# Performance work log

Measured on AMD Instinct MI355X. Metric: run time of the kernel, lower is better.

## Reference

```python
import jax, jax.numpy as jnp
import numpy as np

INPUT_DIM = 64

def setup_inputs() -> dict:
    key = jax.random.key(0)
    k1, k2, k3 = jax.random.split(key, 3)
    B, Lq, Lk, D = 4, 4096, 4096, INPUT_DIM
    return {
        "query": jax.random.normal(k1, (B, Lq, D), dtype=jnp.float32),
        "keys": jax.random.normal(k2, (B, Lk, D), dtype=jnp.float32),
        "values": jax.random.normal(k3, (B, Lk, D), dtype=jnp.float32),
    }

def reference(query, keys, values):
    scale = 1.0 / jnp.sqrt(jnp.asarray(INPUT_DIM, dtype=jnp.float32))
    # scores: [B, Lq, Lk]
    scores = jnp.einsum("bqd,bkd->bqk", query, keys) * scale
    attn = jax.nn.softmax(scores, axis=-1)
    # output: [B, Lq, D]
    return jnp.einsum("bqk,bkd->bqd", attn, values)
```

## Files before the change

kernel.cpp:

```cpp
#include <hip/hip_runtime.h>
#include <hip/hip_bf16.h>

typedef __bf16 bf16x8 __attribute__((ext_vector_type(8)));
typedef float  f32x4  __attribute__((ext_vector_type(4)));

#define LQ 4096
#define LKK 4096
#define DH 64
#define KBLK 64
#define QBLK 64
#define NIT (LKK / KBLK)
#define NB 4
#define GR_TILE 512
#define ARR_ELEMS ((size_t)NB * NIT * GR_TILE * 8)
#define KV_BYTES (4 * ARR_ELEMS * sizeof(__bf16))
#define PO_BYTES ((size_t)512 * 4096 * sizeof(float))
#define PML_BYTES ((size_t)512 * 128 * sizeof(float))
#define WS_SPLIT (KV_BYTES + PO_BYTES + PML_BYTES)
#define WS_SINGLE KV_BYTES

union BFU { unsigned short u; __bf16 b; };
__device__ __forceinline__ __bf16 u2bf(unsigned short v) { BFU x; x.u = v; return x.b; }
__device__ __forceinline__ unsigned short bf2u(__bf16 b) { BFU x; x.b = b; return x.u; }

typedef const __attribute__((address_space(1))) void* gas1_t;
typedef __attribute__((address_space(3))) void* las3_t;
__device__ __forceinline__ void gload_lds16(const void* g, void* l) {
    __builtin_amdgcn_global_load_lds((gas1_t)g, (las3_t)l, 16, 0, 0);
}

__device__ __forceinline__ unsigned cvt_pk_bf16(float a, float b) {
    unsigned r;
    asm volatile("v_cvt_pk_bf16_f32 %0, %1, %2" : "=v"(r) : "v"(a), "v"(b));
    return r;
}


__global__ __launch_bounds__(256)
void prepack(const float* __restrict__ Kg, const float* __restrict__ Vg,
             __bf16* __restrict__ ws)
{
    __bf16* KHI = ws;
    __bf16* KLO = ws + ARR_ELEMS;
    __bf16* VHI = ws + 2 * ARR_ELEMS;
    __bf16* VLO = ws + 3 * ARR_ELEMS;

    const int gid = blockIdx.x * 256 + threadIdx.x;
    const int isV = gid >> 17;
    const int t   = gid & 131071;
    const int b   = t >> 15;
    const int rem = t & 32767;
    const int kt  = rem >> 9;
    const int G   = rem & 511;
    const int blk = G >> 7;
    const int c   = (G >> 6) & 1;
    const int gg  = (G >> 4) & 3;
    const int ll  = G & 15;

    const size_t dst = ((size_t)(b * NIT + kt) * GR_TILE + G) * 8;
    float x[8];
    if (!isV) {
        const float* src = Kg + ((size_t)b * LKK + kt * KBLK + 16 * blk + ll) * DH + 32 * c + 8 * gg;
        float4 a0 = *(const float4*)src;
        float4 a1 = *(const float4*)(src + 4);
        x[0]=a0.x; x[1]=a0.y; x[2]=a0.z; x[3]=a0.w;
        x[4]=a1.x; x[5]=a1.y; x[6]=a1.z; x[7]=a1.w;
        bf16x8 h, l;
#pragma unroll
        for (int j = 0; j < 8; ++j) {
            __bf16 hh = (__bf16)x[j];
            h[j] = hh; l[j] = (__bf16)(x[j] - (float)hh);
        }
        *(bf16x8*)&KHI[dst] = h;  *(bf16x8*)&KLO[dst] = l;
    } else {
        const float* src = Vg + ((size_t)b * LKK + kt * KBLK + 32 * c + 8 * gg) * DH + 16 * blk + ll;
#pragma unroll
        for (int j = 0; j < 8; ++j) x[j] = src[(size_t)j * DH];
        bf16x8 h, l;
#pragma unroll
        for (int j = 0; j < 8; ++j) {
            __bf16 hh = (__bf16)x[j];
            h[j] = hh; l[j] = (__bf16)(x[j] - (float)hh);
        }
        *(bf16x8*)&VHI[dst] = h;  *(bf16x8*)&VLO[dst] = l;
    }
}

__global__ __launch_bounds__(256, 2)
void attn_split(const float* __restrict__ Qg, const __bf16* __restrict__ ws,
                float* __restrict__ PO, float* __restrict__ PML)
{
    const int bid = blockIdx.x;
    const int h   = bid & 1;
    const int bz  = (bid >> 1) & 3;
    const int qt  = bid >> 3;
    const int pb  = h * 256 + bz * 64 + qt;
    const int tid  = threadIdx.x;
    const int w    = tid >> 6;
    const int lane = tid & 63;
    const int g    = lane >> 4;
    const int l15  = lane & 15;
    const int q0   = qt * QBLK + w * 16;

    __shared__ __align__(16) __bf16 TILES[2][4][GR_TILE * 8];
    __shared__ __align__(16) unsigned int PSM[4][16 * 64];

    const __bf16* wsA[4] = { ws, ws + ARR_ELEMS, ws + 2 * ARR_ELEMS, ws + 3 * ARR_ELEMS };
    const size_t bqoff = (size_t)bz * LQ * DH;

    bf16x8 qhi[2], qlo[2];
#pragma unroll
    for (int c = 0; c < 2; ++c) {
        const float* src = Qg + bqoff + (size_t)(q0 + l15) * DH + 32 * c + 8 * g;
#pragma unroll
        for (int j = 0; j < 8; ++j) {
            float x = src[j] * 0.125f;
            __bf16 hh = (__bf16)x;
            qhi[c][j] = hh;
            qlo[c][j] = (__bf16)(x - (float)hh);
        }
    }

    auto STAGE = [&](int buf, int kt) {
        const size_t toff = (size_t)(bz * NIT + kt) * GR_TILE * 8;
#pragma unroll
        for (int a = 0; a < 4; ++a) {
            const __bf16* src = wsA[a] + toff + (size_t)(w * 128 + lane) * 8;
            __bf16* dst = &TILES[buf][a][w * 128 * 8];
            gload_lds16(src, dst);
            gload_lds16(src + 64 * 8, dst + 64 * 8);
        }
    };

    f32x4 oacc[4] = {};
    float m_run = -1e30f, l_run = 0.f;

    const int kt0 = h * (NIT / 2);
    STAGE(0, kt0);
    __syncthreads();

    int cur = 0;
    const int sw = (l15 & 7) << 2;
    const int prow = l15 * 64;

    for (int it = 0; it < NIT / 2; ++it) {
        if (it + 1 < NIT / 2) STAGE(cur ^ 1, kt0 + it + 1);

        const __bf16* KHI_l = TILES[cur][0];
        const __bf16* KLO_l = TILES[cur][1];
        const __bf16* VHI_l = TILES[cur][2];
        const __bf16* VLO_l = TILES[cur][3];

        f32x4 s[4] = {};
        __builtin_amdgcn_s_setprio(1);
#pragma unroll
        for (int kb = 0; kb < 4; ++kb) {
#pragma unroll
            for (int c = 0; c < 2; ++c) {
                bf16x8 kh = *(const bf16x8*)&KHI_l[((kb * 2 + c) * 64 + lane) * 8];
                bf16x8 kl = *(const bf16x8*)&KLO_l[((kb * 2 + c) * 64 + lane) * 8];
                s[kb] = __builtin_amdgcn_mfma_f32_16x16x32_bf16(kh, qhi[c], s[kb], 0, 0, 0);
                s[kb] = __builtin_amdgcn_mfma_f32_16x16x32_bf16(kh, qlo[c], s[kb], 0, 0, 0);
                s[kb] = __builtin_amdgcn_mfma_f32_16x16x32_bf16(kl, qhi[c], s[kb], 0, 0, 0);
            }
        }
        __builtin_amdgcn_s_setprio(0);

        float tmax = -1e30f;
#pragma unroll
        for (int kb = 0; kb < 4; ++kb)
#pragma unroll
            for (int r = 0; r < 4; ++r)
                tmax = fmaxf(tmax, s[kb][r]);
        tmax = fmaxf(tmax, __shfl_xor(tmax, 16, 64));
        tmax = fmaxf(tmax, __shfl_xor(tmax, 32, 64));

        const bool defer = __all(tmax <= m_run + 8.f);
        float alpha = 1.f;
        if (!defer) {
            float mnew = fmaxf(m_run, tmax);
            alpha = __expf(m_run - mnew);
            m_run = mnew;
        }

        float psum = 0.f;
#pragma unroll
        for (int kb = 0; kb < 4; ++kb)
#pragma unroll
            for (int r = 0; r < 4; ++r) {
                float p = __expf(s[kb][r] - m_run);
                s[kb][r] = p;
                psum += p;
            }
        psum += __shfl_xor(psum, 16, 64);
        psum += __shfl_xor(psum, 32, 64);

        if (!defer) {
            l_run = l_run * alpha + psum;
#pragma unroll
            for (int db = 0; db < 4; ++db) oacc[db] *= alpha;
        } else {
            l_run += psum;
        }

#pragma unroll
        for (int kb = 0; kb < 4; ++kb) {
            unsigned h0 = cvt_pk_bf16(s[kb][0], s[kb][1]);
            unsigned h1 = cvt_pk_bf16(s[kb][2], s[kb][3]);
            float l0 = s[kb][0] - __uint_as_float(h0 << 16);
            float l1 = s[kb][1] - __uint_as_float(h0 & 0xffff0000u);
            float l2 = s[kb][2] - __uint_as_float(h1 << 16);
            float l3 = s[kb][3] - __uint_as_float(h1 & 0xffff0000u);
            unsigned lo0 = cvt_pk_bf16(l0, l1);
            unsigned lo1 = cvt_pk_bf16(l2, l3);
            const int wb = 8 * kb + 2 * g;
            PSM[w][prow + ((wb)     ^ sw)]      = h0;
            PSM[w][prow + ((wb + 1) ^ sw)]      = h1;
            PSM[w][prow + 32 + ((wb)     ^ sw)] = lo0;
            PSM[w][prow + 32 + ((wb + 1) ^ sw)] = lo1;
        }

#pragma unroll
        for (int c = 0; c < 2; ++c) {
            const int qb = prow + (((4 * c + g) ^ (l15 & 7)) << 2);
            bf16x8 ph = *(const bf16x8*)&PSM[w][qb];
            bf16x8 pl = *(const bf16x8*)&PSM[w][qb + 32];
            __builtin_amdgcn_s_setprio(1);
#pragma unroll
            for (int db = 0; db < 4; ++db) {
                bf16x8 vh = *(const bf16x8*)&VHI_l[((db * 2 + c) * 64 + lane) * 8];
                bf16x8 vl = *(const bf16x8*)&VLO_l[((db * 2 + c) * 64 + lane) * 8];
                oacc[db] = __builtin_amdgcn_mfma_f32_16x16x32_bf16(vh, ph, oacc[db], 0, 0, 0);
                oacc[db] = __builtin_amdgcn_mfma_f32_16x16x32_bf16(vl, ph, oacc[db], 0, 0, 0);
                oacc[db] = __builtin_amdgcn_mfma_f32_16x16x32_bf16(vh, pl, oacc[db], 0, 0, 0);
            }
            __builtin_amdgcn_s_setprio(0);
        }

        __syncthreads();
        cur ^= 1;
    }

    float* po = PO + (size_t)pb * (QBLK * DH) + (size_t)(w * 16 + l15) * DH;
#pragma unroll
    for (int db = 0; db < 4; ++db)
        *(f32x4*)&po[16 * db + 4 * g] = oacc[db];
    if (g == 0) {
        PML[pb * 128 + w * 16 + l15]      = m_run;
        PML[pb * 128 + 64 + w * 16 + l15] = l_run;
    }
}

__global__ __launch_bounds__(256)
void combine(const float* __restrict__ PO, const float* __restrict__ PML,
             float* __restrict__ Og)
{
    const int t  = blockIdx.x * 256 + threadIdx.x;
    const int d   = t & 63;
    const int row = (t >> 6) & 4095;
    const int bz  = t >> 18;
    const int qt  = row >> 6, ri = row & 63;
    const int pb0 = bz * 64 + qt;
    const int pb1 = 256 + pb0;
    float m0 = PML[pb0 * 128 + ri], l0 = PML[pb0 * 128 + 64 + ri];
    float m1 = PML[pb1 * 128 + ri], l1 = PML[pb1 * 128 + 64 + ri];
    float M  = fmaxf(m0, m1);
    float a0 = __expf(m0 - M), a1 = __expf(m1 - M);
    float o0 = PO[(size_t)pb0 * 4096 + ri * 64 + d];
    float o1 = PO[(size_t)pb1 * 4096 + ri * 64 + d];
    Og[t] = (a0 * o0 + a1 * o1) / (a0 * l0 + a1 * l1);
}

__global__ __launch_bounds__(256, 1)
void attn_fwd_pre(const float* __restrict__ Qg, const __bf16* __restrict__ ws,
                  float* __restrict__ Og)
{
    const int bid = blockIdx.x;
    const int bz  = (bid >> 1) & 3;
    const int qt  = ((bid & 1) << 5) | (bid >> 3);
    const int tid  = threadIdx.x;
    const int w    = tid >> 6;
    const int lane = tid & 63;
    const int g    = lane >> 4;
    const int l15  = lane & 15;
    const int q0   = qt * QBLK + w * 16;

    __shared__ __align__(16) __bf16 TILES[2][4][GR_TILE * 8];
    __shared__ __align__(16) unsigned int PSM[4][16 * 64];

    const __bf16* wsA[4] = { ws, ws + ARR_ELEMS, ws + 2 * ARR_ELEMS, ws + 3 * ARR_ELEMS };
    const size_t bqoff = (size_t)bz * LQ * DH;

    bf16x8 qhi[2], qlo[2];
#pragma unroll
    for (int c = 0; c < 2; ++c) {
        const float* src = Qg + bqoff + (size_t)(q0 + l15) * DH + 32 * c + 8 * g;
#pragma unroll
        for (int j = 0; j < 8; ++j) {
            float x = src[j] * 0.125f;
            __bf16 hh = (__bf16)x;
            qhi[c][j] = hh;
            qlo[c][j] = (__bf16)(x - (float)hh);
        }
    }

    auto STAGE = [&](int buf, int kt) {
        const size_t toff = (size_t)(bz * NIT + kt) * GR_TILE * 8;
#pragma unroll
        for (int a = 0; a < 4; ++a) {
            const __bf16* src = wsA[a] + toff + (size_t)(w * 128 + lane) * 8;
            __bf16* dst = &TILES[buf][a][w * 128 * 8];
            gload_lds16(src, dst);
            gload_lds16(src + 64 * 8, dst + 64 * 8);
        }
    };

    f32x4 oacc[4] = {};
    float m_run[4], l_run[4];
#pragma unroll
    for (int r = 0; r < 4; ++r) { m_run[r] = -1e30f; l_run[r] = 0.f; }

    STAGE(0, 0);
    __syncthreads();

    int cur = 0;
    for (int kt = 0; kt < NIT; ++kt) {
        if (kt + 1 < NIT) STAGE(cur ^ 1, kt + 1);

        const __bf16* KHI_l = TILES[cur][0];
        const __bf16* KLO_l = TILES[cur][1];
        const __bf16* VHI_l = TILES[cur][2];
        const __bf16* VLO_l = TILES[cur][3];

        f32x4 s[4] = {};
#pragma unroll
        for (int kb = 0; kb < 4; ++kb) {
#pragma unroll
            for (int c = 0; c < 2; ++c) {
                bf16x8 kh = *(const bf16x8*)&KHI_l[((kb * 2 + c) * 64 + lane) * 8];
                bf16x8 kl = *(const bf16x8*)&KLO_l[((kb * 2 + c) * 64 + lane) * 8];
                s[kb] = __builtin_amdgcn_mfma_f32_16x16x32_bf16(qhi[c], kh, s[kb], 0, 0, 0);
                s[kb] = __builtin_amdgcn_mfma_f32_16x16x32_bf16(qlo[c], kh, s[kb], 0, 0, 0);
                s[kb] = __builtin_amdgcn_mfma_f32_16x16x32_bf16(qhi[c], kl, s[kb], 0, 0, 0);
            }
        }

        float tmax[4];
#pragma unroll
        for (int r = 0; r < 4; ++r)
            tmax[r] = fmaxf(fmaxf(s[0][r], s[1][r]), fmaxf(s[2][r], s[3][r]));
#pragma unroll
        for (int off = 1; off < 16; off <<= 1)
#pragma unroll
            for (int r = 0; r < 4; ++r)
                tmax[r] = fmaxf(tmax[r], __shfl_xor(tmax[r], off, 64));

        float alpha[4], psum[4];
#pragma unroll
        for (int r = 0; r < 4; ++r) {
            float mnew = fmaxf(m_run[r], tmax[r]);
            alpha[r] = __expf(m_run[r] - mnew);
            m_run[r] = mnew;
            psum[r] = 0.f;
        }
#pragma unroll
        for (int kb = 0; kb < 4; ++kb)
#pragma unroll
            for (int r = 0; r < 4; ++r) {
                float p = __expf(s[kb][r] - m_run[r]);
                s[kb][r] = p;
                psum[r] += p;
            }
#pragma unroll
        for (int off = 1; off < 16; off <<= 1)
#pragma unroll
            for (int r = 0; r < 4; ++r)
                psum[r] += __shfl_xor(psum[r], off, 64);
#pragma unroll
        for (int r = 0; r < 4; ++r) {
            l_run[r] = l_run[r] * alpha[r] + psum[r];
#pragma unroll
            for (int db = 0; db < 4; ++db) oacc[db][r] *= alpha[r];
        }

#pragma unroll
        for (int kb = 0; kb < 4; ++kb)
#pragma unroll
            for (int r = 0; r < 4; ++r) {
                float p = s[kb][r];
                __bf16 hh = (__bf16)p;
                __bf16 ll2 = (__bf16)(p - (float)hh);
                const int row = 4 * g + r;
                const int idx = row * 64 + (((4 * kb + (l15 >> 2) + row) & 15) << 2) + (l15 & 3);
                PSM[w][idx] = (unsigned int)bf2u(hh) | ((unsigned int)bf2u(ll2) << 16);
            }

#pragma unroll
        for (int c = 0; c < 2; ++c) {
            const unsigned int* prow2 = &PSM[w][l15 * 64];
            const int qg = 2 * g + 8 * c;
            uint4 ulo = *(const uint4*)&prow2[((qg + l15) & 15) << 2];
            uint4 uhi = *(const uint4*)&prow2[((qg + 1 + l15) & 15) << 2];
            unsigned int uu[8] = { ulo.x, ulo.y, ulo.z, ulo.w, uhi.x, uhi.y, uhi.z, uhi.w };
            bf16x8 ph, pl;
#pragma unroll
            for (int j = 0; j < 8; ++j) {
                ph[j] = u2bf((unsigned short)(uu[j] & 0xffffu));
                pl[j] = u2bf((unsigned short)(uu[j] >> 16));
            }
#pragma unroll
            for (int db = 0; db < 4; ++db) {
                bf16x8 vh = *(const bf16x8*)&VHI_l[((db * 2 + c) * 64 + lane) * 8];
                bf16x8 vl = *(const bf16x8*)&VLO_l[((db * 2 + c) * 64 + lane) * 8];
                oacc[db] = __builtin_amdgcn_mfma_f32_16x16x32_bf16(ph, vh, oacc[db], 0, 0, 0);
                oacc[db] = __builtin_amdgcn_mfma_f32_16x16x32_bf16(ph, vl, oacc[db], 0, 0, 0);
                oacc[db] = __builtin_amdgcn_mfma_f32_16x16x32_bf16(pl, vh, oacc[db], 0, 0, 0);
            }
        }

        __syncthreads();
        cur ^= 1;
    }

#pragma unroll
    for (int r = 0; r < 4; ++r) {
        float inv = 1.0f / l_run[r];
#pragma unroll
        for (int db = 0; db < 4; ++db)
            Og[bqoff + (size_t)(q0 + 4 * g + r) * DH + 16 * db + l15] = oacc[db][r] * inv;
    }
}

extern "C" void kernel_launch(void* const* d_in, const int* in_sizes, int n_in,
                              void* d_out, int out_size, void* d_ws, size_t ws_size,
                              hipStream_t stream) {
    (void)in_sizes; (void)n_in; (void)out_size;
    const float* Q = (const float*)d_in[0];
    const float* K = (const float*)d_in[1];
    const float* V = (const float*)d_in[2];
    float* O = (float*)d_out;

    if (ws_size >= WS_SPLIT) {
        __bf16* ws = (__bf16*)d_ws;
        float* PO  = (float*)((char*)d_ws + KV_BYTES);
        float* PML = (float*)((char*)d_ws + KV_BYTES + PO_BYTES);
        prepack<<<dim3(1024), dim3(256), 0, stream>>>(K, V, ws);
        attn_split<<<dim3(512), dim3(256), 0, stream>>>(Q, ws, PO, PML);
        combine<<<dim3(4096), dim3(256), 0, stream>>>(PO, PML, O);
    } else if (ws_size >= WS_SINGLE) {
        __bf16* ws = (__bf16*)d_ws;
        prepack<<<dim3(1024), dim3(256), 0, stream>>>(K, V, ws);
        attn_fwd_pre<<<dim3(256), dim3(256), 0, stream>>>(Q, ws, O);
    }
}
```

Measured before the change: 132.7 us.

## Halve key tile, split keys four ways, compute row sums via MFMA

Shrinks the key/value tile from 64 to 32 rows, which halves LDS use and raises launch bounds to four blocks per CU. It splits the key range into four partitions across 1024 blocks, with a templated combine kernel merging the partial results. The per-iteration exp-sum and shuffle reduction is replaced by an extra MFMA against a vector of ones that accumulates the softmax denominator. The cost is more partial-output traffic, a larger combine pass, and twice as many loop iterations and barriers per block.

```diff
diff --git a/kernel.cpp b/kernel.cpp
--- a/kernel.cpp
+++ b/kernel.cpp
@@ -7,21 +7,16 @@
 #define LQ 4096
 #define LKK 4096
 #define DH 64
-#define KBLK 64
+#define KBLK 32
 #define QBLK 64
 #define NIT (LKK / KBLK)
 #define NB 4
-#define GR_TILE 512
+#define GR_TILE 256
 #define ARR_ELEMS ((size_t)NB * NIT * GR_TILE * 8)
 #define KV_BYTES (4 * ARR_ELEMS * sizeof(__bf16))
-#define PO_BYTES ((size_t)512 * 4096 * sizeof(float))
-#define PML_BYTES ((size_t)512 * 128 * sizeof(float))
-#define WS_SPLIT (KV_BYTES + PO_BYTES + PML_BYTES)
-#define WS_SINGLE KV_BYTES
-
-union BFU { unsigned short u; __bf16 b; };
-__device__ __forceinline__ __bf16 u2bf(unsigned short v) { BFU x; x.u = v; return x.b; }
-__device__ __forceinline__ unsigned short bf2u(__bf16 b) { BFU x; x.b = b; return x.u; }
+#define PO_BYTES(N)  ((size_t)(N) * 256 * QBLK * DH * sizeof(float))
+#define PML_BYTES(N) ((size_t)(N) * 256 * 128 * sizeof(float))
+#define WS_N(N) (KV_BYTES + PO_BYTES(N) + PML_BYTES(N))
 
 typedef const __attribute__((address_space(1))) void* gas1_t;
 typedef __attribute__((address_space(3))) void* las3_t;
@@ -50,17 +45,16 @@
     const int t   = gid & 131071;
     const int b   = t >> 15;
     const int rem = t & 32767;
-    const int kt  = rem >> 9;
-    const int G   = rem & 511;
-    const int blk = G >> 7;
-    const int c   = (G >> 6) & 1;
+    const int kt  = rem >> 8;
+    const int G   = rem & 255;
     const int gg  = (G >> 4) & 3;
     const int ll  = G & 15;
 
     const size_t dst = ((size_t)(b * NIT + kt) * GR_TILE + G) * 8;
     float x[8];
     if (!isV) {
-        const float* src = Kg + ((size_t)b * LKK + kt * KBLK + 16 * blk + ll) * DH + 32 * c + 8 * gg;
+        const int kb = G >> 7, c = (G >> 6) & 1;
+        const float* src = Kg + ((size_t)b * LKK + kt * KBLK + 16 * kb + ll) * DH + 32 * c + 8 * gg;
         float4 a0 = *(const float4*)src;
         float4 a1 = *(const float4*)(src + 4);
         x[0]=a0.x; x[1]=a0.y; x[2]=a0.z; x[3]=a0.w;
@@ -73,7 +67,8 @@
         }
         *(bf16x8*)&KHI[dst] = h;  *(bf16x8*)&KLO[dst] = l;
     } else {
-        const float* src = Vg + ((size_t)b * LKK + kt * KBLK + 32 * c + 8 * gg) * DH + 16 * blk + ll;
+        const int db = G >> 6;
+        const float* src = Vg + ((size_t)b * LKK + kt * KBLK + 8 * gg) * DH + 16 * db + ll;
 #pragma unroll
         for (int j = 0; j < 8; ++j) x[j] = src[(size_t)j * DH];
         bf16x8 h, l;
@@ -86,15 +81,18 @@
     }
 }
 
-__global__ __launch_bounds__(256, 2)
-void attn_split(const float* __restrict__ Qg, const __bf16* __restrict__ ws,
-                float* __restrict__ PO, float* __restrict__ PML)
+template<int NSPLIT>
+__global__ __launch_bounds__(256, 4)
+void attn_split_t(const float* __restrict__ Qg, const __bf16* __restrict__ ws,
+                  float* __restrict__ PO, float* __restrict__ PML)
 {
+    constexpr int LS  = (NSPLIT == 4) ? 2 : ((NSPLIT == 2) ? 1 : 0);
+    constexpr int TPB = NIT / NSPLIT;
     const int bid = blockIdx.x;
-    const int h   = bid & 1;
-    const int bz  = (bid >> 1) & 3;
-    const int qt  = bid >> 3;
-    const int pb  = h * 256 + bz * 64 + qt;
+    const int sp  = bid & (NSPLIT - 1);
+    const int bz  = (bid >> LS) & 3;
+    const int qt  = bid >> (LS + 2);
+    const int pb  = sp * 256 + bz * 64 + qt;
     const int tid  = threadIdx.x;
     const int w    = tid >> 6;
     const int lane = tid & 63;
@@ -103,7 +101,7 @@
     const int q0   = qt * QBLK + w * 16;
 
     __shared__ __align__(16) __bf16 TILES[2][4][GR_TILE * 8];
-    __shared__ __align__(16) unsigned int PSM[4][16 * 64];
+    __shared__ __align__(16) unsigned int PSM[4][16][32];
 
     const __bf16* wsA[4] = { ws, ws + ARR_ELEMS, ws + 2 * ARR_ELEMS, ws + 3 * ARR_ELEMS };
     const size_t bqoff = (size_t)bz * LQ * DH;
@@ -120,41 +118,42 @@
             qlo[c][j] = (__bf16)(x - (float)hh);
         }
     }
+    bf16x8 vones;
+#pragma unroll
+    for (int j = 0; j < 8; ++j) vones[j] = (__bf16)1.0f;
 
     auto STAGE = [&](int buf, int kt) {
         const size_t toff = (size_t)(bz * NIT + kt) * GR_TILE * 8;
 #pragma unroll
         for (int a = 0; a < 4; ++a) {
-            const __bf16* src = wsA[a] + toff + (size_t)(w * 128 + lane) * 8;
-            __bf16* dst = &TILES[buf][a][w * 128 * 8];
-            gload_lds16(src, dst);
-            gload_lds16(src + 64 * 8, dst + 64 * 8);
+            const __bf16* src = wsA[a] + toff + (size_t)(w * 64 + lane) * 8;
+            gload_lds16(src, &TILES[buf][a][w * 64 * 8]);
         }
     };
 
     f32x4 oacc[4] = {};
-    float m_run = -1e30f, l_run = 0.f;
-
-    const int kt0 = h * (NIT / 2);
+    f32x4 oext = {};
+    float m_run = -1e30f;
+
+    const int kt0 = sp * TPB;
     STAGE(0, kt0);
     __syncthreads();
 
     int cur = 0;
-    const int sw = (l15 & 7) << 2;
-    const int prow = l15 * 64;
-
-    for (int it = 0; it < NIT / 2; ++it) {
-        if (it + 1 < NIT / 2) STAGE(cur ^ 1, kt0 + it + 1);
+    const int sig = (l15 & 3) ^ (((l15 >> 2) & 3) << 1);
+
+    for (int it = 0; it < TPB; ++it) {
+        if (it + 1 < TPB) STAGE(cur ^ 1, kt0 + it + 1);
 
         const __bf16* KHI_l = TILES[cur][0];
         const __bf16* KLO_l = TILES[cur][1];
         const __bf16* VHI_l = TILES[cur][2];
         const __bf16* VLO_l = TILES[cur][3];
 
-        f32x4 s[4] = {};
+        f32x4 s[2] = {};
         __builtin_amdgcn_s_setprio(1);
 #pragma unroll
-        for (int kb = 0; kb < 4; ++kb) {
+        for (int kb = 0; kb < 2; ++kb) {
 #pragma unroll
             for (int c = 0; c < 2; ++c) {
                 bf16x8 kh = *(const bf16x8*)&KHI_l[((kb * 2 + c) * 64 + lane) * 8];
@@ -166,45 +165,29 @@
         }
         __builtin_amdgcn_s_setprio(0);
 
-        float tmax = -1e30f;
-#pragma unroll
-        for (int kb = 0; kb < 4; ++kb)
-#pragma unroll
-            for (int r = 0; r < 4; ++r)
-                tmax = fmaxf(tmax, s[kb][r]);
+        float tmax = fmaxf(fmaxf(fmaxf(s[0][0], s[0][1]), fmaxf(s[0][2], s[0][3])),
+                           fmaxf(fmaxf(s[1][0], s[1][1]), fmaxf(s[1][2], s[1][3])));
         tmax = fmaxf(tmax, __shfl_xor(tmax, 16, 64));
         tmax = fmaxf(tmax, __shfl_xor(tmax, 32, 64));
 
         const bool defer = __all(tmax <= m_run + 8.f);
-        float alpha = 1.f;
         if (!defer) {
             float mnew = fmaxf(m_run, tmax);
-            alpha = __expf(m_run - mnew);
+            float alpha = __expf(m_run - mnew);
             m_run = mnew;
-        }
-
-        float psum = 0.f;
-#pragma unroll
-        for (int kb = 0; kb < 4; ++kb)
-#pragma unroll
-            for (int r = 0; r < 4; ++r) {
-                float p = __expf(s[kb][r] - m_run);
-                s[kb][r] = p;
-                psum += p;
-            }
-        psum += __shfl_xor(psum, 16, 64);
-        psum += __shfl_xor(psum, 32, 64);
-
-        if (!defer) {
-            l_run = l_run * alpha + psum;
 #pragma unroll
             for (int db = 0; db < 4; ++db) oacc[db] *= alpha;
-        } else {
-            l_run += psum;
-        }
-
-#pragma unroll
-        for (int kb = 0; kb < 4; ++kb) {
+            oext *= alpha;
+        }
+
+#pragma unroll
+        for (int kb = 0; kb < 2; ++kb)
+#pragma unroll
+            for (int r = 0; r < 4; ++r)
+                s[kb][r] = __expf(s[kb][r] - m_run);
+
+#pragma unroll
+        for (int kb = 0; kb < 2; ++kb) {
             unsigned h0 = cvt_pk_bf16(s[kb][0], s[kb][1]);
             unsigned h1 = cvt_pk_bf16(s[kb][2], s[kb][3]);
             float l0 = s[kb][0] - __uint_as_float(h0 << 16);
@@ -213,27 +196,28 @@
             float l3 = s[kb][3] - __uint_as_float(h1 & 0xffff0000u);
             unsigned lo0 = cvt_pk_bf16(l0, l1);
             unsigned lo1 = cvt_pk_bf16(l2, l3);
-            const int wb = 8 * kb + 2 * g;
-            PSM[w][prow + ((wb)     ^ sw)]      = h0;
-            PSM[w][prow + ((wb + 1) ^ sw)]      = h1;
-            PSM[w][prow + 32 + ((wb)     ^ sw)] = lo0;
-            PSM[w][prow + 32 + ((wb + 1) ^ sw)] = lo1;
-        }
-
-#pragma unroll
-        for (int c = 0; c < 2; ++c) {
-            const int qb = prow + (((4 * c + g) ^ (l15 & 7)) << 2);
-            bf16x8 ph = *(const bf16x8*)&PSM[w][qb];
-            bf16x8 pl = *(const bf16x8*)&PSM[w][qb + 32];
+            const int base = ((( (2 * kb + (g >> 1)) ^ sig) << 2) | ((g & 1) << 1));
+            uint2 hh; hh.x = h0;  hh.y = h1;
+            uint2 ll; ll.x = lo0; ll.y = lo1;
+            *(uint2*)&PSM[w][l15][base]      = hh;
+            *(uint2*)&PSM[w][l15][base ^ 16] = ll;
+        }
+
+        {
+            const int rbase = (g ^ sig) << 2;
+            bf16x8 ph = *(const bf16x8*)&PSM[w][l15][rbase];
+            bf16x8 pl = *(const bf16x8*)&PSM[w][l15][rbase ^ 16];
             __builtin_amdgcn_s_setprio(1);
 #pragma unroll
             for (int db = 0; db < 4; ++db) {
-                bf16x8 vh = *(const bf16x8*)&VHI_l[((db * 2 + c) * 64 + lane) * 8];
-                bf16x8 vl = *(const bf16x8*)&VLO_l[((db * 2 + c) * 64 + lane) * 8];
+                bf16x8 vh = *(const bf16x8*)&VHI_l[(db * 64 + lane) * 8];
+                bf16x8 vl = *(const bf16x8*)&VLO_l[(db * 64 + lane) * 8];
                 oacc[db] = __builtin_amdgcn_mfma_f32_16x16x32_bf16(vh, ph, oacc[db], 0, 0, 0);
                 oacc[db] = __builtin_amdgcn_mfma_f32_16x16x32_bf16(vl, ph, oacc[db], 0, 0, 0);
                 oacc[db] = __builtin_amdgcn_mfma_f32_16x16x32_bf16(vh, pl, oacc[db], 0, 0, 0);
             }
+            oext = __builtin_amdgcn_mfma_f32_16x16x32_bf16(vones, ph, oext, 0, 0, 0);
+            oext = __builtin_amdgcn_mfma_f32_16x16x32_bf16(vones, pl, oext, 0, 0, 0);
             __builtin_amdgcn_s_setprio(0);
         }
 
@@ -241,194 +225,54 @@
         cur ^= 1;
     }
 
-    float* po = PO + (size_t)pb * (QBLK * DH) + (size_t)(w * 16 + l15) * DH;
-#pragma unroll
-    for (int db = 0; db < 4; ++db)
-        *(f32x4*)&po[16 * db + 4 * g] = oacc[db];
-    if (g == 0) {
-        PML[pb * 128 + w * 16 + l15]      = m_run;
-        PML[pb * 128 + 64 + w * 16 + l15] = l_run;
-    }
-}
-
+    if constexpr (NSPLIT == 1) {
+        float inv = 1.0f / oext[0];
+        float* og = PO + bqoff + (size_t)(q0 + l15) * DH;
+#pragma unroll
+        for (int db = 0; db < 4; ++db) {
+            f32x4 v = oacc[db] * inv;
+            *(f32x4*)&og[16 * db + 4 * g] = v;
+        }
+    } else {
+        float* po = PO + (size_t)pb * (QBLK * DH) + (size_t)(w * 16 + l15) * DH;
+#pragma unroll
+        for (int db = 0; db < 4; ++db)
+            *(f32x4*)&po[16 * db + 4 * g] = oacc[db];
+        if (g == 0) {
+            PML[pb * 128 + w * 16 + l15]      = m_run;
+            PML[pb * 128 + 64 + w * 16 + l15] = oext[0];
+        }
+    }
+}
+
+template<int NSPLIT>
 __global__ __launch_bounds__(256)
-void combine(const float* __restrict__ PO, const float* __restrict__ PML,
-             float* __restrict__ Og)
+void combine_t(const float* __restrict__ PO, const float* __restrict__ PML,
+               float* __restrict__ Og)
 {
-    const int t  = blockIdx.x * 256 + threadIdx.x;
+    const int t   = blockIdx.x * 256 + threadIdx.x;
     const int d   = t & 63;
     const int row = (t >> 6) & 4095;
     const int bz  = t >> 18;
     const int qt  = row >> 6, ri = row & 63;
-    const int pb0 = bz * 64 + qt;
-    const int pb1 = 256 + pb0;
-    float m0 = PML[pb0 * 128 + ri], l0 = PML[pb0 * 128 + 64 + ri];
-    float m1 = PML[pb1 * 128 + ri], l1 = PML[pb1 * 128 + 64 + ri];
-    float M  = fmaxf(m0, m1);
-    float a0 = __expf(m0 - M), a1 = __expf(m1 - M);
-    float o0 = PO[(size_t)pb0 * 4096 + ri * 64 + d];
-    float o1 = PO[(size_t)pb1 * 4096 + ri * 64 + d];
-    Og[t] = (a0 * o0 + a1 * o1) / (a0 * l0 + a1 * l1);
-}
-
-__global__ __launch_bounds__(256, 1)
-void attn_fwd_pre(const float* __restrict__ Qg, const __bf16* __restrict__ ws,
-                  float* __restrict__ Og)
-{
-    const int bid = blockIdx.x;
-    const int bz  = (bid >> 1) & 3;
-    const int qt  = ((bid & 1) << 5) | (bid >> 3);
-    const int tid  = threadIdx.x;
-    const int w    = tid >> 6;
-    const int lane = tid & 63;
-    const int g    = lane >> 4;
-    const int l15  = lane & 15;
-    const int q0   = qt * QBLK + w * 16;
-
-    __shared__ __align__(16) __bf16 TILES[2][4][GR_TILE * 8];
-    __shared__ __align__(16) unsigned int PSM[4][16 * 64];
-
-    const __bf16* wsA[4] = { ws, ws + ARR_ELEMS, ws + 2 * ARR_ELEMS, ws + 3 * ARR_ELEMS };
-    const size_t bqoff = (size_t)bz * LQ * DH;
-
-    bf16x8 qhi[2], qlo[2];
-#pragma unroll
-    for (int c = 0; c < 2; ++c) {
-        const float* src = Qg + bqoff + (size_t)(q0 + l15) * DH + 32 * c + 8 * g;
-#pragma unroll
-        for (int j = 0; j < 8; ++j) {
-            float x = src[j] * 0.125f;
-            __bf16 hh = (__bf16)x;
-            qhi[c][j] = hh;
-            qlo[c][j] = (__bf16)(x - (float)hh);
-        }
-    }
-
-    auto STAGE = [&](int buf, int kt) {
-        const size_t toff = (size_t)(bz * NIT + kt) * GR_TILE * 8;
-#pragma unroll
-        for (int a = 0; a < 4; ++a) {
-            const __bf16* src = wsA[a] + toff + (size_t)(w * 128 + lane) * 8;
-            __bf16* dst = &TILES[buf][a][w * 128 * 8];
-            gload_lds16(src, dst);
-            gload_lds16(src + 64 * 8, dst + 64 * 8);
-        }
-    };
-
-    f32x4 oacc[4] = {};
-    float m_run[4], l_run[4];
-#pragma unroll
-    for (int r = 0; r < 4; ++r) { m_run[r] = -1e30f; l_run[r] = 0.f; }
-
-    STAGE(0, 0);
-    __syncthreads();
-
-    int cur = 0;
-    for (int kt = 0; kt < NIT; ++kt) {
-        if (kt + 1 < NIT) STAGE(cur ^ 1, kt + 1);
-
-        const __bf16* KHI_l = TILES[cur][0];
-        const __bf16* KLO_l = TILES[cur][1];
-        const __bf16* VHI_l = TILES[cur][2];
-        const __bf16* VLO_l = TILES[cur][3];
-
-        f32x4 s[4] = {};
-#pragma unroll
-        for (int kb = 0; kb < 4; ++kb) {
-#pragma unroll
-            for (int c = 0; c < 2; ++c) {
-                bf16x8 kh = *(const bf16x8*)&KHI_l[((kb * 2 + c) * 64 + lane) * 8];
-                bf16x8 kl = *(const bf16x8*)&KLO_l[((kb * 2 + c) * 64 + lane) * 8];
-                s[kb] = __builtin_amdgcn_mfma_f32_16x16x32_bf16(qhi[c], kh, s[kb], 0, 0, 0);
-                s[kb] = __builtin_amdgcn_mfma_f32_16x16x32_bf16(qlo[c], kh, s[kb], 0, 0, 0);
-                s[kb] = __builtin_amdgcn_mfma_f32_16x16x32_bf16(qhi[c], kl, s[kb], 0, 0, 0);
-            }
-        }
-
-        float tmax[4];
-#pragma unroll
-        for (int r = 0; r < 4; ++r)
-            tmax[r] = fmaxf(fmaxf(s[0][r], s[1][r]), fmaxf(s[2][r], s[3][r]));
-#pragma unroll
-        for (int off = 1; off < 16; off <<= 1)
-#pragma unroll
-            for (int r = 0; r < 4; ++r)
-                tmax[r] = fmaxf(tmax[r], __shfl_xor(tmax[r], off, 64));
-
-        float alpha[4], psum[4];
-#pragma unroll
-        for (int r = 0; r < 4; ++r) {
-            float mnew = fmaxf(m_run[r], tmax[r]);
-            alpha[r] = __expf(m_run[r] - mnew);
-            m_run[r] = mnew;
-            psum[r] = 0.f;
-        }
-#pragma unroll
-        for (int kb = 0; kb < 4; ++kb)
-#pragma unroll
-            for (int r = 0; r < 4; ++r) {
-                float p = __expf(s[kb][r] - m_run[r]);
-                s[kb][r] = p;
-                psum[r] += p;
-            }
-#pragma unroll
-        for (int off = 1; off < 16; off <<= 1)
-#pragma unroll
-            for (int r = 0; r < 4; ++r)
-                psum[r] += __shfl_xor(psum[r], off, 64);
-#pragma unroll
-        for (int r = 0; r < 4; ++r) {
-            l_run[r] = l_run[r] * alpha[r] + psum[r];
-#pragma unroll
-            for (int db = 0; db < 4; ++db) oacc[db][r] *= alpha[r];
-        }
-
-#pragma unroll
-        for (int kb = 0; kb < 4; ++kb)
-#pragma unroll
-            for (int r = 0; r < 4; ++r) {
-                float p = s[kb][r];
-                __bf16 hh = (__bf16)p;
-                __bf16 ll2 = (__bf16)(p - (float)hh);
-                const int row = 4 * g + r;
-                const int idx = row * 64 + (((4 * kb + (l15 >> 2) + row) & 15) << 2) + (l15 & 3);
-                PSM[w][idx] = (unsigned int)bf2u(hh) | ((unsigned int)bf2u(ll2) << 16);
-            }
-
-#pragma unroll
-        for (int c = 0; c < 2; ++c) {
-            const unsigned int* prow2 = &PSM[w][l15 * 64];
-            const int qg = 2 * g + 8 * c;
-            uint4 ulo = *(const uint4*)&prow2[((qg + l15) & 15) << 2];
-            uint4 uhi = *(const uint4*)&prow2[((qg + 1 + l15) & 15) << 2];
-            unsigned int uu[8] = { ulo.x, ulo.y, ulo.z, ulo.w, uhi.x, uhi.y, uhi.z, uhi.w };
-            bf16x8 ph, pl;
-#pragma unroll
-            for (int j = 0; j < 8; ++j) {
-                ph[j] = u2bf((unsigned short)(uu[j] & 0xffffu));
-                pl[j] = u2bf((unsigned short)(uu[j] >> 16));
-            }
-#pragma unroll
-            for (int db = 0; db < 4; ++db) {
-                bf16x8 vh = *(const bf16x8*)&VHI_l[((db * 2 + c) * 64 + lane) * 8];
-                bf16x8 vl = *(const bf16x8*)&VLO_l[((db * 2 + c) * 64 + lane) * 8];
-                oacc[db] = __builtin_amdgcn_mfma_f32_16x16x32_bf16(ph, vh, oacc[db], 0, 0, 0);
-                oacc[db] = __builtin_amdgcn_mfma_f32_16x16x32_bf16(ph, vl, oacc[db], 0, 0, 0);
-                oacc[db] = __builtin_amdgcn_mfma_f32_16x16x32_bf16(pl, vh, oacc[db], 0, 0, 0);
-            }
-        }
-
-        __syncthreads();
-        cur ^= 1;
-    }
-
-#pragma unroll
-    for (int r = 0; r < 4; ++r) {
-        float inv = 1.0f / l_run[r];
-#pragma unroll
-        for (int db = 0; db < 4; ++db)
-            Og[bqoff + (size_t)(q0 + 4 * g + r) * DH + 16 * db + l15] = oacc[db][r] * inv;
-    }
+    float m[NSPLIT], l[NSPLIT], o[NSPLIT];
+    float M = -1e30f;
+#pragma unroll
+    for (int i = 0; i < NSPLIT; ++i) {
+        const int pbi = i * 256 + bz * 64 + qt;
+        m[i] = PML[pbi * 128 + ri];
+        l[i] = PML[pbi * 128 + 64 + ri];
+        o[i] = PO[(size_t)pbi * 4096 + ri * 64 + d];
+        M = fmaxf(M, m[i]);
+    }
+    float num = 0.f, den = 0.f;
+#pragma unroll
+    for (int i = 0; i < NSPLIT; ++i) {
+        float a = __expf(m[i] - M);
+        num += a * o[i];
+        den += a * l[i];
+    }
+    Og[t] = num / den;
 }
 
 extern "C" void kernel_launch(void* const* d_in, const int* in_sizes, int n_in,
@@ -439,17 +283,21 @@
     const float* K = (const float*)d_in[1];
     const float* V = (const float*)d_in[2];
     float* O = (float*)d_out;
-
-    if (ws_size >= WS_SPLIT) {
-        __bf16* ws = (__bf16*)d_ws;
+    __bf16* ws = (__bf16*)d_ws;
+
+    prepack<<<dim3(1024), dim3(256), 0, stream>>>(K, V, ws);
+
+    if (ws_size >= WS_N(4)) {
         float* PO  = (float*)((char*)d_ws + KV_BYTES);
-        float* PML = (float*)((char*)d_ws + KV_BYTES + PO_BYTES);
-        prepack<<<dim3(1024), dim3(256), 0, stream>>>(K, V, ws);
-        attn_split<<<dim3(512), dim3(256), 0, stream>>>(Q, ws, PO, PML);
-        combine<<<dim3(4096), dim3(256), 0, stream>>>(PO, PML, O);
-    } else if (ws_size >= WS_SINGLE) {
-        __bf16* ws = (__bf16*)d_ws;
-        prepack<<<dim3(1024), dim3(256), 0, stream>>>(K, V, ws);
-        attn_fwd_pre<<<dim3(256), dim3(256), 0, stream>>>(Q, ws, O);
-    }
-}
+        float* PML = (float*)((char*)d_ws + KV_BYTES + PO_BYTES(4));
+        attn_split_t<4><<<dim3(1024), dim3(256), 0, stream>>>(Q, ws, PO, PML);
+        combine_t<4><<<dim3(4096), dim3(256), 0, stream>>>(PO, PML, O);
+    } else if (ws_size >= WS_N(2)) {
+        float* PO  = (float*)((char*)d_ws + KV_BYTES);
+        float* PML = (float*)((char*)d_ws + KV_BYTES + PO_BYTES(2));
+        attn_split_t<2><<<dim3(512), dim3(256), 0, stream>>>(Q, ws, PO, PML);
+        combine_t<2><<<dim3(4096), dim3(256), 0, stream>>>(PO, PML, O);
+    } else {
+        attn_split_t<1><<<dim3(256), dim3(256), 0, stream>>>(Q, ws, O, nullptr);
+    }
+}
```

New measurement: 135.7 us. +2.3%, slower.
